# Performance work log

Hardware: AMD Instinct MI355X
Metric: run time of the kernel (lower is better)

The kernel has to match this reference:

```python
import jax, jax.numpy as jnp
import numpy as np

B, S, HID = 2, 4096, 2048
H, D, R = 4, 64, 32  # num_index_heads, head_dim, rope_head_dim
LN_EPS = 1e-5


def rotate_half(x):
    x1, x2 = jnp.split(x, 2, axis=-1)
    return jnp.concatenate([-x2, x1], axis=-1)


def setup_inputs() -> dict:
    key = jax.random.key(0)
    ks = jax.random.split(key, 8)
    hidden_states = jax.random.normal(ks[0], (B, S, HID), jnp.float32)
    cos = jax.random.uniform(ks[1], (B, S, R), jnp.float32)
    sin = jax.random.uniform(ks[2], (B, S, R), jnp.float32)
    Wq = jax.random.normal(ks[3], (HID, H * D), jnp.float32) * 0.02
    Wk = jax.random.normal(ks[4], (HID, D), jnp.float32) * 0.02
    Ww = jax.random.normal(ks[5], (HID, H), jnp.float32) * 0.02
    ln_gamma = jnp.ones((D,), jnp.float32)
    ln_beta = jnp.zeros((D,), jnp.float32)
    return {"hidden_states": hidden_states, "cos": cos, "sin": sin,
            "Wq": Wq, "Wk": Wk, "Ww": Ww,
            "ln_gamma": ln_gamma, "ln_beta": ln_beta}


def reference(hidden_states, cos, sin, Wq, Wk, Ww, ln_gamma, ln_beta):
    b, s, _ = hidden_states.shape
    h = Ww.shape[1]
    d = Wk.shape[1]
    r = cos.shape[-1]

    # projections
    q = (hidden_states @ Wq).reshape(b, s, h, d)      # [B,S,H,D]
    k = hidden_states @ Wk                             # [B,S,D]
    w = hidden_states @ Ww                             # [B,S,H]

    # LayerNorm on k over head_dim
    mu = jnp.mean(k, axis=-1, keepdims=True)
    var = jnp.mean(jnp.square(k - mu), axis=-1, keepdims=True)
    k = (k - mu) * jax.lax.rsqrt(var + LN_EPS) * ln_gamma + ln_beta

    # partial RoPE on first r dims
    q_pe, q_nope = q[..., :r], q[..., r:]
    k_pe, k_nope = k[..., :r], k[..., r:]
    cos_q = cos[:, :, None, :]
    sin_q = sin[:, :, None, :]
    q_pe = q_pe * cos_q + rotate_half(q_pe) * sin_q
    k_pe = k_pe * cos + rotate_half(k_pe) * sin
    q = jnp.concatenate([q_pe, q_nope], axis=-1)       # [B,S,H,D]
    k = jnp.concatenate([k_pe, k_nope], axis=-1)       # [B,S,D]

    # relu(q k^T), single shared key head broadcast over index heads
    score = jax.nn.relu(jnp.einsum('bqhd,bkd->bhqk', q, k))  # [B,H,Sq,Sk]
    # per-query, per-head weights, summed over heads
    indexer_score = jnp.einsum('bqh,bhqk->bqk', w, score)    # [B,Sq,Sk]
    return indexer_score
```

## Files before the change

kernel.cpp:

```cpp
#include <hip/hip_runtime.h>

#define BDIM 2
#define SDIM 4096
#define HIDDEN 2048
#define NH 4
#define DD 64
#define RR 32
constexpr float LN_EPS = 1e-5f;

typedef _Float16 half8 __attribute__((ext_vector_type(8)));
typedef __attribute__((ext_vector_type(4))) float f32x4;

__device__ __forceinline__ void gload_lds16(const void* g, void* l) {
    __builtin_amdgcn_global_load_lds(
        (const __attribute__((address_space(1))) void*)g,
        (__attribute__((address_space(3))) void*)l, 16, 0, 0);
}

__global__ __launch_bounds__(256) void split_hs(
    const float* __restrict__ hs, _Float16* __restrict__ hs2)
{
    const int idx  = blockIdx.x * 256 + threadIdx.x;
    const int m    = idx >> 8;
    const int slot = idx & 255;
    const float4 v0 = *reinterpret_cast<const float4*>(&hs[(size_t)m * HIDDEN + slot * 8]);
    const float4 v1 = *reinterpret_cast<const float4*>(&hs[(size_t)m * HIDDEN + slot * 8 + 4]);
    _Float16 o[8];
    o[0] = (_Float16)v0.x; o[1] = (_Float16)v0.y;
    o[2] = (_Float16)v0.z; o[3] = (_Float16)v0.w;
    o[4] = (_Float16)v1.x; o[5] = (_Float16)v1.y;
    o[6] = (_Float16)v1.z; o[7] = (_Float16)v1.w;
    const int eoff = (slot * 8) ^ ((m & 7) << 3);
    *reinterpret_cast<half8*>(&hs2[(size_t)m * HIDDEN + eoff]) =
        *reinterpret_cast<half8*>(o);
}

__global__ __launch_bounds__(256) void prep_w2(
    const float* __restrict__ Wq, const float* __restrict__ Wk,
    const float* __restrict__ Ww, _Float16* __restrict__ Wt2)
{
    __shared__ float T[64][65];
    const int k0 = blockIdx.x * 64, n0 = blockIdx.y * 64;
    const int tid = threadIdx.x;
    {
        const int kr = tid >> 2;
        const int nq = (tid & 3) * 16;
        const int gk = k0 + kr;
        #pragma unroll
        for (int c = 0; c < 16; ++c) {
            const int n = n0 + nq + c;
            float v;
            if (n < 256)      v = Wq[(size_t)gk * 256 + n];
            else if (n < 320) v = Wk[(size_t)gk * 64 + (n - 256)];
            else if (n < 324) v = Ww[(size_t)gk * NH + (n - 320)];
            else              v = 0.f;
            T[kr][nq + c] = v;
        }
    }
    __syncthreads();
    {
        const int nr = tid >> 2;
        const int kc = (tid & 3) * 16;
        const int n  = n0 + nr;
        #pragma unroll
        for (int s = 0; s < 2; ++s) {
            const int kb = kc + s * 8;
            _Float16 e[8];
            #pragma unroll
            for (int t = 0; t < 8; ++t) e[t] = (_Float16)T[kb + t][nr];
            const int eoff = (k0 + kb) ^ ((nr & 7) << 3);
            *reinterpret_cast<half8*>(&Wt2[(size_t)n * HIDDEN + eoff]) =
                *reinterpret_cast<half8*>(e);
        }
    }
}

__global__ __launch_bounds__(256) void proj_mfma(
    const _Float16* __restrict__ hs2, const _Float16* __restrict__ Wt2,
    const float* __restrict__ cosb, const float* __restrict__ sinb,
    const float* __restrict__ gamma, const float* __restrict__ beta,
    _Float16* __restrict__ qout, _Float16* __restrict__ kout,
    float* __restrict__ wout)
{
    __shared__ _Float16 Asm[128 * 128];
    __shared__ _Float16 Bsm[64 * 128];

    const int m0   = blockIdx.x * 128;
    const int ng   = blockIdx.y;
    const int tid  = threadIdx.x;
    const int wave = tid >> 6, lane = tid & 63;
    const int lr = lane & 15, lh = lane >> 4;

    f32x4 acc[2][4];
    #pragma unroll
    for (int i = 0; i < 2; ++i)
        #pragma unroll
        for (int j = 0; j < 4; ++j)
            acc[i][j] = (f32x4){0.f, 0.f, 0.f, 0.f};

    const int srow  = tid >> 4;
    const int sslot = tid & 15;
    const _Float16* gA = hs2 + (size_t)(m0 + srow) * HIDDEN + sslot * 8;
    const _Float16* gB = Wt2 + (size_t)(ng * 64 + srow) * HIDDEN + sslot * 8;
    _Float16* lA = Asm + tid * 8;
    _Float16* lB = Bsm + tid * 8;

    for (int k0 = 0; k0 < HIDDEN; k0 += 128) {
        #pragma unroll
        for (int i = 0; i < 8; ++i)
            gload_lds16(gA + (size_t)i * 16 * HIDDEN + k0, lA + i * 2048);
        #pragma unroll
        for (int i = 0; i < 4; ++i)
            gload_lds16(gB + (size_t)i * 16 * HIDDEN + k0, lB + i * 2048);
        __syncthreads();

        #pragma unroll
        for (int kk = 0; kk < 4; ++kk) {
            half8 av[2], bv[4];
            #pragma unroll
            for (int i = 0; i < 2; ++i) {
                const int row = wave * 32 + i * 16 + lr;
                const int off = (row * 128 + kk * 32 + lh * 8) ^ ((row & 7) << 3);
                av[i] = *reinterpret_cast<const half8*>(&Asm[off]);
            }
            #pragma unroll
            for (int j = 0; j < 4; ++j) {
                const int row = j * 16 + lr;
                const int off = (row * 128 + kk * 32 + lh * 8) ^ ((row & 7) << 3);
                bv[j] = *reinterpret_cast<const half8*>(&Bsm[off]);
            }
            #pragma unroll
            for (int i = 0; i < 2; ++i)
                #pragma unroll
                for (int j = 0; j < 4; ++j)
                    acc[i][j] = __builtin_amdgcn_mfma_f32_16x16x32_f16(
                        av[i], bv[j], acc[i][j], 0, 0, 0);
        }
        __syncthreads();
    }

    if (ng < 4) {
        #pragma unroll
        for (int i = 0; i < 2; ++i)
            #pragma unroll
            for (int r = 0; r < 4; ++r) {
                const int m = m0 + wave * 32 + i * 16 + lh * 4 + r;
                const float x0 = acc[i][0][r], x1 = acc[i][1][r];
                const float c0 = cosb[(size_t)m * RR + lr];
                const float s0 = sinb[(size_t)m * RR + lr];
                const float c1 = cosb[(size_t)m * RR + 16 + lr];
                const float s1 = sinb[(size_t)m * RR + 16 + lr];
                const int sw = (m & 7) << 3;
                const size_t rowb = (size_t)m * (NH * DD);
                const int e0 = ng * DD + lr;
                qout[rowb + (e0 ^ sw)]        = (_Float16)(x0 * c0 - x1 * s0);
                qout[rowb + ((e0 + 16) ^ sw)] = (_Float16)(x1 * c1 + x0 * s1);
                qout[rowb + ((e0 + 32) ^ sw)] = (_Float16)acc[i][2][r];
                qout[rowb + ((e0 + 48) ^ sw)] = (_Float16)acc[i][3][r];
            }
    } else if (ng == 4) {
        float g[4], bb[4];
        #pragma unroll
        for (int j = 0; j < 4; ++j) { g[j] = gamma[j * 16 + lr]; bb[j] = beta[j * 16 + lr]; }
        #pragma unroll
        for (int i = 0; i < 2; ++i)
            #pragma unroll
            for (int r = 0; r < 4; ++r) {
                float t1 = 0.f, t2 = 0.f;
                #pragma unroll
                for (int j = 0; j < 4; ++j) {
                    const float a = acc[i][j][r];
                    t1 += a; t2 += a * a;
                }
                #pragma unroll
                for (int msk = 1; msk < 16; msk <<= 1) {
                    t1 += __shfl_xor(t1, msk, 64);
                    t2 += __shfl_xor(t2, msk, 64);
                }
                const float mu  = t1 * (1.f / 64.f);
                const float var = t2 * (1.f / 64.f) - mu * mu;
                const float rs  = rsqrtf(var + LN_EPS);
                const int m = m0 + wave * 32 + i * 16 + lh * 4 + r;
                float x[4];
                #pragma unroll
                for (int j = 0; j < 4; ++j)
                    x[j] = (acc[i][j][r] - mu) * rs * g[j] + bb[j];
                const float c0 = cosb[(size_t)m * RR + lr];
                const float s0 = sinb[(size_t)m * RR + lr];
                const float c1 = cosb[(size_t)m * RR + 16 + lr];
                const float s1 = sinb[(size_t)m * RR + 16 + lr];
                const float y0 = x[0] * c0 - x[1] * s0;
                const float y1 = x[1] * c1 + x[0] * s1;
                const size_t base = (size_t)m * DD + lr;
                kout[base]      = (_Float16)y0;
                kout[base + 16] = (_Float16)y1;
                kout[base + 32] = (_Float16)x[2];
                kout[base + 48] = (_Float16)x[3];
            }
    } else {
        if (lr < NH) {
            #pragma unroll
            for (int i = 0; i < 2; ++i)
                #pragma unroll
                for (int r = 0; r < 4; ++r) {
                    const int m = m0 + wave * 32 + i * 16 + lh * 4 + r;
                    wout[(size_t)m * NH + lr] = acc[i][0][r];
                }
        }
    }
}

__global__ __launch_bounds__(256) void score_kernel(
    const _Float16* __restrict__ qb, const _Float16* __restrict__ kb,
    const float* __restrict__ wr, float* __restrict__ out)
{
    __shared__ _Float16 Qlds[64 * 256];
    __shared__ float Wlds[64 * 4];

    const int kc  = blockIdx.x;
    const int q0  = blockIdx.y * 64;
    const int b   = blockIdx.z;
    const int tid = threadIdx.x;
    const int wave = tid >> 6, lane = tid & 63;
    const int wm = wave >> 1, wn = wave & 1;
    const int lr = lane & 15, lh = lane >> 4;
    const int kbase = kc * 512;

    #pragma unroll
    for (int i = 0; i < 8; ++i) {
        const int id   = i * 256 + tid;
        const int row  = id >> 5;
        const int slot = id & 31;
        gload_lds16(qb + (size_t)(b * SDIM + q0 + row) * 256 + slot * 8,
                    Qlds + id * 8);
    }
    Wlds[tid] = wr[(size_t)(b * SDIM + q0) * NH + tid];
    __syncthreads();

    f32x4 wreg[2][4];
    #pragma unroll
    for (int i = 0; i < 2; ++i)
        #pragma unroll
        for (int r = 0; r < 4; ++r) {
            const int row = wm * 32 + i * 16 + lh * 4 + r;
            wreg[i][r] = *reinterpret_cast<const f32x4*>(&Wlds[row * 4]);
        }

    const size_t krow_base = (size_t)(b * SDIM + kbase + wn * 32);
    #define LOADK(dst, st)                                                      \
        _Pragma("unroll")                                                       \
        for (int j = 0; j < 2; ++j)                                             \
            _Pragma("unroll")                                                   \
            for (int ks = 0; ks < 2; ++ks)                                      \
                dst[j][ks] = *reinterpret_cast<const half8*>(                   \
                    &kb[(krow_base + (st) * 64 + j * 16 + lr) * DD + ks * 32 + lh * 8]);

    half8 kcur[2][2], knx[2][2];
    LOADK(kcur, 0)

    for (int st = 0; st < 8; ++st) {
        if (st < 7) { LOADK(knx, st + 1) }

        f32x4 o[2][2];
        #pragma unroll
        for (int i = 0; i < 2; ++i)
            #pragma unroll
            for (int j = 0; j < 2; ++j)
                o[i][j] = (f32x4){0.f, 0.f, 0.f, 0.f};

        #pragma unroll
        for (int h = 0; h < NH; ++h) {
            half8 qf[2][2];
            #pragma unroll
            for (int i = 0; i < 2; ++i)
                #pragma unroll
                for (int ks = 0; ks < 2; ++ks) {
                    const int row  = wm * 32 + i * 16 + lr;
                    const int slot = (h * 8 + ks * 4 + lh) ^ (row & 7);
                    qf[i][ks] = *reinterpret_cast<const half8*>(
                        &Qlds[row * 256 + slot * 8]);
                }
            f32x4 s[2][2];
            #pragma unroll
            for (int i = 0; i < 2; ++i)
                #pragma unroll
                for (int j = 0; j < 2; ++j)
                    s[i][j] = (f32x4){0.f, 0.f, 0.f, 0.f};
            #pragma unroll
            for (int ks = 0; ks < 2; ++ks)
                #pragma unroll
                for (int i = 0; i < 2; ++i)
                    #pragma unroll
                    for (int j = 0; j < 2; ++j)
                        s[i][j] = __builtin_amdgcn_mfma_f32_16x16x32_f16(
                            qf[i][ks], kcur[j][ks], s[i][j], 0, 0, 0);
            #pragma unroll
            for (int i = 0; i < 2; ++i)
                #pragma unroll
                for (int j = 0; j < 2; ++j)
                    #pragma unroll
                    for (int r = 0; r < 4; ++r)
                        o[i][j][r] += wreg[i][r][h] * fmaxf(s[i][j][r], 0.f);
        }

        #pragma unroll
        for (int i = 0; i < 2; ++i)
            #pragma unroll
            for (int r = 0; r < 4; ++r)
                #pragma unroll
                for (int j = 0; j < 2; ++j)
                    out[(size_t)(b * SDIM + q0 + wm * 32 + i * 16 + lh * 4 + r) * SDIM
                        + kbase + st * 64 + wn * 32 + j * 16 + lr] = o[i][j][r];

        #pragma unroll
        for (int j = 0; j < 2; ++j)
            #pragma unroll
            for (int ks = 0; ks < 2; ++ks)
                kcur[j][ks] = knx[j][ks];
    }
    #undef LOADK
}

extern "C" void kernel_launch(void* const* d_in, const int* in_sizes, int n_in,
                              void* d_out, int out_size, void* d_ws, size_t ws_size,
                              hipStream_t stream) {
    const float* hs    = (const float*)d_in[0];
    const float* cosb  = (const float*)d_in[1];
    const float* sinb  = (const float*)d_in[2];
    const float* Wq    = (const float*)d_in[3];
    const float* Wk    = (const float*)d_in[4];
    const float* Ww    = (const float*)d_in[5];
    const float* gamma = (const float*)d_in[6];
    const float* beta  = (const float*)d_in[7];
    float* out = (float*)d_out;

    _Float16* hs2 = (_Float16*)d_out;

    char* wsb = (char*)d_ws;
    _Float16* qb  = (_Float16*)wsb;
    _Float16* kb  = (_Float16*)(wsb + (size_t)BDIM * SDIM * 256 * 2);
    float*    ww  = (float*)(wsb + (size_t)BDIM * SDIM * 256 * 2
                                  + (size_t)BDIM * SDIM * DD * 2);
    _Float16* Wt2 = (_Float16*)(wsb + (size_t)BDIM * SDIM * 256 * 2
                                     + (size_t)BDIM * SDIM * DD * 2
                                     + (size_t)BDIM * SDIM * NH * 4);

    prep_w2<<<dim3(HIDDEN / 64, 6), 256, 0, stream>>>(Wq, Wk, Ww, Wt2);

    split_hs<<<(BDIM * SDIM * (HIDDEN / 8)) / 256, 256, 0, stream>>>(hs, hs2);

    proj_mfma<<<dim3((BDIM * SDIM) / 128, 6), 256, 0, stream>>>(
        hs2, Wt2, cosb, sinb, gamma, beta, qb, kb, ww);

    score_kernel<<<dim3(SDIM / 512, SDIM / 64, BDIM), 256, 0, stream>>>(
        qb, kb, ww, out);
}
```

Before: 85.63 us.

## Retile projection GEMM into two 192-column groups with double-buffered LDS

The projection GEMM switches from six 64-column N groups over 128-row tiles to two 192-column groups over 64-row tiles, and the weight layout is padded so Q and K/W columns split cleanly between groups. This cuts redundant re-reads of the hidden-state A tile (read by 2 groups instead of 6) and drops the all-padding W group. It also adds a double-buffered K loop with 64-wide steps, so the next tile's global-to-LDS load overlaps the current MFMAs. The cost is more accumulator registers per wave and a more intricate epilogue that routes each accumulator to the Q, K-layernorm or W output.

Result: slower. 101.8 us (+18.9%).

```diff
diff --git a/kernel.cpp b/kernel.cpp
--- a/kernel.cpp
+++ b/kernel.cpp
@@ -6,6 +6,7 @@
 #define NH 4
 #define DD 64
 #define RR 32
+#define NG_COLS 192
 constexpr float LN_EPS = 1e-5f;
 
 typedef _Float16 half8 __attribute__((ext_vector_type(8)));
@@ -51,8 +52,9 @@
             const int n = n0 + nq + c;
             float v;
             if (n < 256)      v = Wq[(size_t)gk * 256 + n];
-            else if (n < 320) v = Wk[(size_t)gk * 64 + (n - 256)];
-            else if (n < 324) v = Ww[(size_t)gk * NH + (n - 320)];
+            else if (n < 288) v = 0.f;
+            else if (n < 352) v = Wk[(size_t)gk * 64 + (n - 288)];
+            else if (n < 356) v = Ww[(size_t)gk * NH + (n - 352)];
             else              v = 0.f;
             T[kr][nq + c] = v;
         }
@@ -82,130 +84,162 @@
     _Float16* __restrict__ qout, _Float16* __restrict__ kout,
     float* __restrict__ wout)
 {
-    __shared__ _Float16 Asm[128 * 128];
-    __shared__ _Float16 Bsm[64 * 128];
-
-    const int m0   = blockIdx.x * 128;
+    __shared__ _Float16 Asm[2][64 * 64];
+    __shared__ _Float16 Bsm[2][NG_COLS * 64];
+
+    const int m0   = blockIdx.x * 64;
     const int ng   = blockIdx.y;
     const int tid  = threadIdx.x;
     const int wave = tid >> 6, lane = tid & 63;
+    const int wm = wave >> 1, wn = wave & 1;
     const int lr = lane & 15, lh = lane >> 4;
 
-    f32x4 acc[2][4];
+    f32x4 acc[2][6];
     #pragma unroll
     for (int i = 0; i < 2; ++i)
         #pragma unroll
-        for (int j = 0; j < 4; ++j)
+        for (int j = 0; j < 6; ++j)
             acc[i][j] = (f32x4){0.f, 0.f, 0.f, 0.f};
 
-    const int srow  = tid >> 4;
-    const int sslot = tid & 15;
-    const _Float16* gA = hs2 + (size_t)(m0 + srow) * HIDDEN + sslot * 8;
-    const _Float16* gB = Wt2 + (size_t)(ng * 64 + srow) * HIDDEN + sslot * 8;
-    _Float16* lA = Asm + tid * 8;
-    _Float16* lB = Bsm + tid * 8;
-
-    for (int k0 = 0; k0 < HIDDEN; k0 += 128) {
-        #pragma unroll
-        for (int i = 0; i < 8; ++i)
-            gload_lds16(gA + (size_t)i * 16 * HIDDEN + k0, lA + i * 2048);
-        #pragma unroll
-        for (int i = 0; i < 4; ++i)
-            gload_lds16(gB + (size_t)i * 16 * HIDDEN + k0, lB + i * 2048);
-        __syncthreads();
-
-        #pragma unroll
-        for (int kk = 0; kk < 4; ++kk) {
-            half8 av[2], bv[4];
+    #define STAGE(pp, kk) do {                                                  \
+        _Pragma("unroll")                                                       \
+        for (int s2 = 0; s2 < 2; ++s2) {                                        \
+            const int slot = tid + s2 * 256;                                    \
+            gload_lds16(hs2 + (size_t)(m0 + (slot >> 3)) * HIDDEN               \
+                            + (slot & 7) * 8 + (kk),                            \
+                        &Asm[pp][slot * 8]);                                    \
+        }                                                                       \
+        _Pragma("unroll")                                                       \
+        for (int s6 = 0; s6 < 6; ++s6) {                                        \
+            const int slot = tid + s6 * 256;                                    \
+            gload_lds16(Wt2 + (size_t)(ng * NG_COLS + (slot >> 3)) * HIDDEN     \
+                            + (slot & 7) * 8 + (kk),                            \
+                        &Bsm[pp][slot * 8]);                                    \
+        }                                                                       \
+    } while (0)
+
+    STAGE(0, 0);
+    __syncthreads();
+
+    int p = 0;
+    for (int t = 0; t < HIDDEN / 64; ++t) {
+        if (t < HIDDEN / 64 - 1) STAGE(p ^ 1, (t + 1) * 64);
+
+        #pragma unroll
+        for (int ks = 0; ks < 2; ++ks) {
+            half8 av[2], bv[6];
             #pragma unroll
             for (int i = 0; i < 2; ++i) {
-                const int row = wave * 32 + i * 16 + lr;
-                const int off = (row * 128 + kk * 32 + lh * 8) ^ ((row & 7) << 3);
-                av[i] = *reinterpret_cast<const half8*>(&Asm[off]);
-            }
-            #pragma unroll
-            for (int j = 0; j < 4; ++j) {
-                const int row = j * 16 + lr;
-                const int off = (row * 128 + kk * 32 + lh * 8) ^ ((row & 7) << 3);
-                bv[j] = *reinterpret_cast<const half8*>(&Bsm[off]);
-            }
-            #pragma unroll
-            for (int i = 0; i < 2; ++i)
-                #pragma unroll
-                for (int j = 0; j < 4; ++j)
+                const int arow = wm * 32 + i * 16 + lr;
+                const int aoff = (arow * 64 + ks * 32 + lh * 8) ^ ((arow & 7) << 3);
+                av[i] = *reinterpret_cast<const half8*>(&Asm[p][aoff]);
+            }
+            #pragma unroll
+            for (int j = 0; j < 6; ++j) {
+                const int brow = wn * 96 + j * 16 + lr;
+                const int boff = (brow * 64 + ks * 32 + lh * 8) ^ ((brow & 7) << 3);
+                bv[j] = *reinterpret_cast<const half8*>(&Bsm[p][boff]);
+            }
+            #pragma unroll
+            for (int i = 0; i < 2; ++i)
+                #pragma unroll
+                for (int j = 0; j < 6; ++j)
                     acc[i][j] = __builtin_amdgcn_mfma_f32_16x16x32_f16(
                         av[i], bv[j], acc[i][j], 0, 0, 0);
         }
         __syncthreads();
-    }
-
-    if (ng < 4) {
+        p ^= 1;
+    }
+    #undef STAGE
+
+    auto store_q = [&](int j, int basec) {
         #pragma unroll
         for (int i = 0; i < 2; ++i)
             #pragma unroll
             for (int r = 0; r < 4; ++r) {
-                const int m = m0 + wave * 32 + i * 16 + lh * 4 + r;
-                const float x0 = acc[i][0][r], x1 = acc[i][1][r];
+                const int m = m0 + wm * 32 + i * 16 + lh * 4 + r;
+                const int sw = (m & 7) << 3;
+                qout[(size_t)m * 256 + ((basec + lr) ^ sw)] = (_Float16)acc[i][j][r];
+            }
+    };
+    auto store_q_rope = [&](int j, int basec) {
+        #pragma unroll
+        for (int i = 0; i < 2; ++i)
+            #pragma unroll
+            for (int r = 0; r < 4; ++r) {
+                const int m = m0 + wm * 32 + i * 16 + lh * 4 + r;
+                const float x0 = acc[i][j][r], x1 = acc[i][j + 1][r];
                 const float c0 = cosb[(size_t)m * RR + lr];
                 const float s0 = sinb[(size_t)m * RR + lr];
                 const float c1 = cosb[(size_t)m * RR + 16 + lr];
                 const float s1 = sinb[(size_t)m * RR + 16 + lr];
                 const int sw = (m & 7) << 3;
-                const size_t rowb = (size_t)m * (NH * DD);
-                const int e0 = ng * DD + lr;
-                qout[rowb + (e0 ^ sw)]        = (_Float16)(x0 * c0 - x1 * s0);
-                qout[rowb + ((e0 + 16) ^ sw)] = (_Float16)(x1 * c1 + x0 * s1);
-                qout[rowb + ((e0 + 32) ^ sw)] = (_Float16)acc[i][2][r];
-                qout[rowb + ((e0 + 48) ^ sw)] = (_Float16)acc[i][3][r];
-            }
-    } else if (ng == 4) {
-        float g[4], bb[4];
-        #pragma unroll
-        for (int j = 0; j < 4; ++j) { g[j] = gamma[j * 16 + lr]; bb[j] = beta[j * 16 + lr]; }
-        #pragma unroll
-        for (int i = 0; i < 2; ++i)
-            #pragma unroll
-            for (int r = 0; r < 4; ++r) {
-                float t1 = 0.f, t2 = 0.f;
-                #pragma unroll
-                for (int j = 0; j < 4; ++j) {
-                    const float a = acc[i][j][r];
-                    t1 += a; t2 += a * a;
+                const size_t rowb = (size_t)m * 256;
+                qout[rowb + ((basec + lr) ^ sw)]      = (_Float16)(x0 * c0 - x1 * s0);
+                qout[rowb + ((basec + 16 + lr) ^ sw)] = (_Float16)(x1 * c1 + x0 * s1);
+            }
+    };
+
+    if (ng == 0) {
+        if (wn == 0) {
+            store_q_rope(0, 0);  store_q(2, 32);  store_q(3, 48);  store_q_rope(4, 64);
+        } else {
+            store_q(0, 96);  store_q(1, 112);  store_q_rope(2, 128);
+            store_q(4, 160); store_q(5, 176);
+        }
+    } else {
+        if (wn == 0) {
+            store_q_rope(0, 192);  store_q(2, 224);  store_q(3, 240);
+        } else {
+            float g[4], bb[4];
+            #pragma unroll
+            for (int jj = 0; jj < 4; ++jj) {
+                g[jj] = gamma[jj * 16 + lr]; bb[jj] = beta[jj * 16 + lr];
+            }
+            #pragma unroll
+            for (int i = 0; i < 2; ++i)
+                #pragma unroll
+                for (int r = 0; r < 4; ++r) {
+                    float t1 = 0.f, t2 = 0.f;
+                    #pragma unroll
+                    for (int jj = 0; jj < 4; ++jj) {
+                        const float a = acc[i][jj][r];
+                        t1 += a; t2 += a * a;
+                    }
+                    #pragma unroll
+                    for (int msk = 1; msk < 16; msk <<= 1) {
+                        t1 += __shfl_xor(t1, msk, 64);
+                        t2 += __shfl_xor(t2, msk, 64);
+                    }
+                    const float mu  = t1 * (1.f / 64.f);
+                    const float var = t2 * (1.f / 64.f) - mu * mu;
+                    const float rs  = rsqrtf(var + LN_EPS);
+                    const int m = m0 + wm * 32 + i * 16 + lh * 4 + r;
+                    float x[4];
+                    #pragma unroll
+                    for (int jj = 0; jj < 4; ++jj)
+                        x[jj] = (acc[i][jj][r] - mu) * rs * g[jj] + bb[jj];
+                    const float c0 = cosb[(size_t)m * RR + lr];
+                    const float s0 = sinb[(size_t)m * RR + lr];
+                    const float c1 = cosb[(size_t)m * RR + 16 + lr];
+                    const float s1 = sinb[(size_t)m * RR + 16 + lr];
+                    const float y0 = x[0] * c0 - x[1] * s0;
+                    const float y1 = x[1] * c1 + x[0] * s1;
+                    const size_t base = (size_t)m * DD + lr;
+                    kout[base]      = (_Float16)y0;
+                    kout[base + 16] = (_Float16)y1;
+                    kout[base + 32] = (_Float16)x[2];
+                    kout[base + 48] = (_Float16)x[3];
                 }
-                #pragma unroll
-                for (int msk = 1; msk < 16; msk <<= 1) {
-                    t1 += __shfl_xor(t1, msk, 64);
-                    t2 += __shfl_xor(t2, msk, 64);
-                }
-                const float mu  = t1 * (1.f / 64.f);
-                const float var = t2 * (1.f / 64.f) - mu * mu;
-                const float rs  = rsqrtf(var + LN_EPS);
-                const int m = m0 + wave * 32 + i * 16 + lh * 4 + r;
-                float x[4];
-                #pragma unroll
-                for (int j = 0; j < 4; ++j)
-                    x[j] = (acc[i][j][r] - mu) * rs * g[j] + bb[j];
-                const float c0 = cosb[(size_t)m * RR + lr];
-                const float s0 = sinb[(size_t)m * RR + lr];
-                const float c1 = cosb[(size_t)m * RR + 16 + lr];
-                const float s1 = sinb[(size_t)m * RR + 16 + lr];
-                const float y0 = x[0] * c0 - x[1] * s0;
-                const float y1 = x[1] * c1 + x[0] * s1;
-                const size_t base = (size_t)m * DD + lr;
-                kout[base]      = (_Float16)y0;
-                kout[base + 16] = (_Float16)y1;
-                kout[base + 32] = (_Float16)x[2];
-                kout[base + 48] = (_Float16)x[3];
-            }
-    } else {
-        if (lr < NH) {
-            #pragma unroll
-            for (int i = 0; i < 2; ++i)
-                #pragma unroll
-                for (int r = 0; r < 4; ++r) {
-                    const int m = m0 + wave * 32 + i * 16 + lh * 4 + r;
-                    wout[(size_t)m * NH + lr] = acc[i][0][r];
-                }
+            if (lr < NH) {
+                #pragma unroll
+                for (int i = 0; i < 2; ++i)
+                    #pragma unroll
+                    for (int r = 0; r < 4; ++r) {
+                        const int m = m0 + wm * 32 + i * 16 + lh * 4 + r;
+                        wout[(size_t)m * NH + lr] = acc[i][4][r];
+                    }
+            }
         }
     }
 }
@@ -228,10 +262,8 @@
 
     #pragma unroll
     for (int i = 0; i < 8; ++i) {
-        const int id   = i * 256 + tid;
-        const int row  = id >> 5;
-        const int slot = id & 31;
-        gload_lds16(qb + (size_t)(b * SDIM + q0 + row) * 256 + slot * 8,
+        const int id = i * 256 + tid;
+        gload_lds16(qb + (size_t)(b * SDIM + q0 + (id >> 5)) * 256 + (id & 31) * 8,
                     Qlds + id * 8);
     }
     Wlds[tid] = wr[(size_t)(b * SDIM + q0) * NH + tid];
@@ -241,10 +273,9 @@
     #pragma unroll
     for (int i = 0; i < 2; ++i)
         #pragma unroll
-        for (int r = 0; r < 4; ++r) {
-            const int row = wm * 32 + i * 16 + lh * 4 + r;
-            wreg[i][r] = *reinterpret_cast<const f32x4*>(&Wlds[row * 4]);
-        }
+        for (int r = 0; r < 4; ++r)
+            wreg[i][r] = *reinterpret_cast<const f32x4*>(
+                &Wlds[(wm * 32 + i * 16 + lh * 4 + r) * 4]);
 
     const size_t krow_base = (size_t)(b * SDIM + kbase + wn * 32);
     #define LOADK(dst, st)                                                      \
@@ -349,7 +380,7 @@
 
     split_hs<<<(BDIM * SDIM * (HIDDEN / 8)) / 256, 256, 0, stream>>>(hs, hs2);
 
-    proj_mfma<<<dim3((BDIM * SDIM) / 128, 6), 256, 0, stream>>>(
+    proj_mfma<<<dim3((BDIM * SDIM) / 64, 2), 256, 0, stream>>>(
         hs2, Wt2, cosb, sinb, gamma, beta, qb, kb, ww);
 
     score_kernel<<<dim3(SDIM / 512, SDIM / 64, BDIM), 256, 0, stream>>>(
```
